# Kernel optimization log

Measured on AMD Instinct MI355X. Metric: run time of the kernel, lower is better.

The kernel has to match this reference:

```python
import jax, jax.numpy as jnp
import numpy as np

N_MEL = 80
PRENET = 256
ENC = 512
ARNN = 1024
DRNN = 1024
ATT = 128
NF = 32
K = 31
B, S, T = 16, 256, 400


def _lstm_cell(x, h, c, Wih, Whh, bih, bhh):
    # torch nn.LSTMCell math: gates ordered i, f, g, o
    z = x @ Wih.T + bih + h @ Whh.T + bhh
    i, f, g, o = jnp.split(z, 4, axis=-1)
    c_new = jax.nn.sigmoid(f) * c + jax.nn.sigmoid(i) * jnp.tanh(g)
    h_new = jax.nn.sigmoid(o) * jnp.tanh(c_new)
    return h_new, c_new


def setup_inputs() -> dict:
    key = jax.random.key(0)
    ks = jax.random.split(key, 24)
    g = lambda i, shape: (jax.random.normal(ks[i], shape, jnp.float32) * 0.02)
    inp = {
        'memory': jax.random.normal(ks[0], (B, S, ENC), jnp.float32),
        'decoder_inputs': jax.random.normal(ks[1], (B, N_MEL, T), jnp.float32),
        # prenet (LinearNorm, no bias in tacotron2 prenet)
        'Wpre1': g(2, (PRENET, N_MEL)),
        'Wpre2': g(3, (PRENET, PRENET)),
        # attention LSTMCell: input = prenet + enc = 256 + 512 = 768
        'Wih_a': g(4, (4 * ARNN, PRENET + ENC)),
        'Whh_a': g(5, (4 * ARNN, ARNN)),
        'bih_a': jnp.zeros((4 * ARNN,), jnp.float32),
        'bhh_a': jnp.zeros((4 * ARNN,), jnp.float32),
        # location-sensitive attention
        'Wq': g(6, (ATT, ARNN)),
        'Wm': g(7, (ATT, ENC)),
        'v': g(8, (ATT,)),
        'Wloc_conv': g(9, (NF, 2, K)),
        'Wloc_dense': g(10, (ATT, NF)),
        # decoder LSTMCell: input = att_rnn + enc = 1024 + 512 = 1536
        'Wih_d': g(11, (4 * DRNN, ARNN + ENC)),
        'Whh_d': g(12, (4 * DRNN, DRNN)),
        'bih_d': jnp.zeros((4 * DRNN,), jnp.float32),
        'bhh_d': jnp.zeros((4 * DRNN,), jnp.float32),
        # projections from [decoder_hidden ; context] = 1536
        'Wproj': g(13, (N_MEL, DRNN + ENC)),
        'bproj': jnp.zeros((N_MEL,), jnp.float32),
        'Wgate': g(14, (1, DRNN + ENC)),
        'bgate': jnp.zeros((1,), jnp.float32),
        'memory_lengths': jax.random.randint(ks[15], (B,), S // 2, S + 1),
    }
    return inp


def reference(memory, decoder_inputs, Wpre1, Wpre2, Wih_a, Whh_a, bih_a, bhh_a,
              Wq, Wm, v, Wloc_conv, Wloc_dense, Wih_d, Whh_d, bih_d, bhh_d,
              Wproj, bproj, Wgate, bgate, memory_lengths):
    # pad mask: True where position is beyond the encoder length
    pad_mask = jnp.arange(S)[None, :] >= memory_lengths[:, None]  # [B,S]
    proc_mem = memory @ Wm.T  # [B,S,ATT], memory_layer precomputed once

    # parse_decoder_inputs + go frame: [B,80,T] -> [T,B,80], prepend zeros
    di = jnp.transpose(decoder_inputs, (2, 0, 1))
    di = jnp.concatenate([jnp.zeros((1, B, N_MEL), di.dtype), di], axis=0)
    # prenet (dropout treated as identity for deterministic reference)
    pre = jax.nn.relu(jax.nn.relu(di @ Wpre1.T) @ Wpre2.T)  # [T+1,B,256]
    xs = pre[:-1]  # loop consumes indices 0..T-1

    carry0 = (jnp.zeros((B, ARNN)), jnp.zeros((B, ARNN)),
              jnp.zeros((B, DRNN)), jnp.zeros((B, DRNN)),
              jnp.zeros((B, S)), jnp.zeros((B, S)), jnp.zeros((B, ENC)))

    def step(carry, x):
        ah, ac, dh, dc, aw, awc, ctx = carry
        ah, ac = _lstm_cell(jnp.concatenate([x, ctx], -1), ah, ac,
                            Wih_a, Whh_a, bih_a, bhh_a)
        # location features from [prev_weights ; cum_weights]
        awcat = jnp.stack([aw, awc], axis=1)  # [B,2,S]
        loc = jax.lax.conv_general_dilated(
            awcat, Wloc_conv, (1,), ((K // 2, K // 2),),
            dimension_numbers=('NCH', 'OIH', 'NCH'))  # [B,NF,S]
        proc_att = jnp.einsum('bfs,af->bsa', loc, Wloc_dense)  # [B,S,ATT]
        q = ah @ Wq.T  # [B,ATT]
        e = jnp.tanh(q[:, None, :] + proc_att + proc_mem) @ v  # [B,S]
        e = jnp.where(pad_mask, -1e9, e)
        aw = jax.nn.softmax(e, axis=-1)
        ctx = jnp.einsum('bs,bse->be', aw, memory)  # [B,ENC]
        awc = awc + aw
        dh, dc = _lstm_cell(jnp.concatenate([ah, ctx], -1), dh, dc,
                            Wih_d, Whh_d, bih_d, bhh_d)
        hac = jnp.concatenate([dh, ctx], -1)  # [B,1536]
        mel = hac @ Wproj.T + bproj  # [B,80]
        gate = (hac @ Wgate.T + bgate)[:, 0]  # [B]
        return (ah, ac, dh, dc, aw, awc, ctx), (mel, gate, aw)

    _, (mels, gates, aligns) = jax.lax.scan(step, carry0, xs)
    mel_outputs = jnp.transpose(mels, (1, 2, 0))  # [B,80,T]
    gate_outputs = gates.T  # [B,T]
    alignments = jnp.transpose(aligns, (1, 0, 2))  # [B,T,S]
    return mel_outputs, gate_outputs, alignments
```

## Files before the change

### kernel.cpp

```cpp
#include <hip/hip_runtime.h>

typedef unsigned short ushort_t;
typedef unsigned int uint_t;
typedef float f32x4_t __attribute__((ext_vector_type(4)));
typedef short bf16x8_t __attribute__((ext_vector_type(8)));

#define NBATCH 16
#define SMEM   256
#define TSTEPS 400

#define F_XSB   0u
#define F_PM    819200u
#define F_MMIX  1343488u
#define F_W1T   1675264u
#define F_W2T   1695744u
#define F_AHB   1761280u
#define F_DHB   1777664u
#define F_CTXB  1794048u
#define F_DHF   1802240u
#define F_AWG   1835008u
#define F_FLG   1851392u
#define ZERO_BASE  F_AHB
#define ZERO_COUNT 95616u

#define AHF  0
#define CTXF 64
#define DHFL 192
#define AWF  320
#define PRF  336

#define A_AH    0
#define A_CTX   32768
#define A_XS    49152
#define A_RED   57344
#define D_AH    0
#define D_CTX   32768
#define D_DH    49152
#define D_MEMU  81920
#define D_COMB  114688
#define D_AWSM  120832
#define D_PART  121856
#define T_AH    0
#define T_LOCU  32768
#define T_QSM   53248
#define T_VSM   53760
#define T_ESM   54272
#define T_RED   55296
#define T_SMAW  55424
#define T_SMAWC 56448
#define P_DHP   0
#define P_AWP   65536
#define SMEM_BYTES 123904

struct Ptrs {
  const float *memory, *dec_in, *Wpre1, *Wpre2, *Wih_a, *Whh_a, *bih_a, *bhh_a,
              *Wq, *Wm, *v, *Wc, *Wld, *Wih_d, *Whh_d, *bih_d, *bhh_d,
              *Wproj, *bproj, *Wgate, *bgate;
  const int *mlen;
  float *ws;
  float *out;
};

__device__ __forceinline__ float ftanh(float x) {
  float e = __expf(2.f * x);
  return 1.f - 2.f / (e + 1.f);
}
__device__ __forceinline__ float fsig(float x) { return 1.f / (1.f + __expf(-x)); }

__device__ __forceinline__ unsigned f2bfbits(float x) {
  unsigned u = __builtin_bit_cast(unsigned, x);
  return (u + 0x7FFFu + ((u >> 16) & 1u)) >> 16;
}
__device__ __forceinline__ float bf2f(ushort_t u) {
  unsigned v = ((unsigned)u) << 16;
  return __builtin_bit_cast(float, v);
}
__device__ __forceinline__ bf16x8_t packbf8(const float* f) {
  bf16x8_t r;
#pragma unroll
  for (int j = 0; j < 8; ++j) r[j] = (short)f2bfbits(f[j]);
  return r;
}
__device__ __forceinline__ bf16x8_t pack_from_f4(const float* src) {
  const float4* s4 = (const float4*)src;
  float4 lo = s4[0], hi = s4[1];
  float tmp[8] = {lo.x, lo.y, lo.z, lo.w, hi.x, hi.y, hi.z, hi.w};
  return packbf8(tmp);
}
__device__ __forceinline__ bf16x8_t ldbf8(const ushort_t* p) {
  return *(const bf16x8_t*)p;
}
__device__ __forceinline__ unsigned long long ldull_a(const unsigned long long* p) {
  return __hip_atomic_load(p, __ATOMIC_RELAXED, __HIP_MEMORY_SCOPE_AGENT);
}
__device__ __forceinline__ void stull_a(unsigned long long* p, unsigned long long v) {
  __hip_atomic_store(p, v, __ATOMIC_RELAXED, __HIP_MEMORY_SCOPE_AGENT);
}
__device__ __forceinline__ void stf_a(float* p, float v) {
  __hip_atomic_store(p, v, __ATOMIC_RELAXED, __HIP_MEMORY_SCOPE_AGENT);
}
__device__ __forceinline__ float ldf_a(const float* p) {
  return __hip_atomic_load(p, __ATOMIC_RELAXED, __HIP_MEMORY_SCOPE_AGENT);
}
__device__ __forceinline__ void pollge(int* flg, int slot, int thr) {
  while (__hip_atomic_load(flg + slot * 16, __ATOMIC_RELAXED, __HIP_MEMORY_SCOPE_AGENT) < thr)
    __builtin_amdgcn_s_sleep(1);
}
__device__ __forceinline__ void sig(int* flg, int slot, int val) {
  __hip_atomic_store(flg + slot * 16, val, __ATOMIC_RELAXED, __HIP_MEMORY_SCOPE_AGENT);
}
__device__ __forceinline__ void lds_st8(char* smc, int base, int row, int row_sh,
                                        int bytecol, unsigned long long v) {
  *(unsigned long long*)(smc + base + (row << row_sh) + (bytecol ^ ((row & 7) << 4))) = v;
}
__device__ __forceinline__ bf16x8_t lds_bf8(const char* smc, int base, int row,
                                            int row_sh, int bytecol) {
  return *(const bf16x8_t*)(smc + base + (row << row_sh) + (bytecol ^ ((row & 7) << 4)));
}
#define MFMA16(a,b,c) __builtin_amdgcn_mfma_f32_16x16x32_bf16((a),(b),(c),0,0,0)

__global__ __launch_bounds__(256) void k_zero(Ptrs p) {
  unsigned i = blockIdx.x * 256 + threadIdx.x;
  if (i < ZERO_COUNT) p.ws[ZERO_BASE + i] = 0.f;
}

__global__ __launch_bounds__(256) void k_transpose(Ptrs p) {
  int i = blockIdx.x * 256 + threadIdx.x;
  if (i < 20480) {
    int m = i >> 8, c = i & 255;
    p.ws[F_W1T + i] = p.Wpre1[c * 80 + m];
  } else if (i < 20480 + 65536) {
    int j = i - 20480;
    int pp = j >> 8, q = j & 255;
    p.ws[F_W2T + j] = p.Wpre2[q * 256 + pp];
  }
}

__global__ __launch_bounds__(256) void k_prenet(Ptrs p) {
  __shared__ float dil[NBATCH * 80];
  __shared__ float h1[NBATCH * 256];
  const int t = blockIdx.x, tid = threadIdx.x;
  const float* W1T = p.ws + F_W1T;
  const float* W2T = p.ws + F_W2T;

  for (int i = tid; i < NBATCH * 80; i += 256) {
    int b = i / 80, m = i - b * 80;
    dil[i] = (t == 0) ? 0.f : p.dec_in[((size_t)b * 80 + m) * 400 + (t - 1)];
  }
  __syncthreads();

  float acc[NBATCH];
#pragma unroll
  for (int b = 0; b < NBATCH; ++b) acc[b] = 0.f;
  for (int m = 0; m < 80; ++m) {
    float w = W1T[m * 256 + tid];
#pragma unroll
    for (int b = 0; b < NBATCH; ++b) acc[b] = fmaf(dil[b * 80 + m], w, acc[b]);
  }
#pragma unroll
  for (int b = 0; b < NBATCH; ++b) h1[b * 256 + tid] = fmaxf(acc[b], 0.f);
  __syncthreads();

#pragma unroll
  for (int b = 0; b < NBATCH; ++b) acc[b] = 0.f;
  for (int q = 0; q < 256; ++q) {
    float w = W2T[q * 256 + tid];
#pragma unroll
    for (int b = 0; b < NBATCH; ++b) acc[b] = fmaf(h1[b * 256 + q], w, acc[b]);
  }
  ushort_t* xsbU = (ushort_t*)(p.ws + F_XSB);
#pragma unroll
  for (int b = 0; b < NBATCH; ++b)
    xsbU[((size_t)(t * NBATCH + b)) * 256 + tid] = (ushort_t)f2bfbits(fmaxf(acc[b], 0.f));
}

__global__ __launch_bounds__(256) void k_packwq(Ptrs p) {
  int s = blockIdx.x * 256 + threadIdx.x;
  if (s >= 16384) return;
  int m16s = s & 15, kqs = (s >> 4) & 3, c = (s >> 6) & 31, w = s >> 11;
  int r = w * 16 + m16s, col = c * 32 + kqs * 8;
  ushort_t* wqp = (ushort_t*)(p.ws + F_W1T);
  bf16x8_t f = pack_from_f4(p.Wq + (size_t)r * 1024 + col);
  *(bf16x8_t*)(wqp + (size_t)s * 8) = f;
}

__global__ __launch_bounds__(256) void k_procmem(Ptrs p) {
  __shared__ alignas(16) float msl[16 * 512];
  const int b = blockIdx.x >> 4, s0 = (blockIdx.x & 15) << 4;
  const int tid = threadIdx.x;
  const float4* src = (const float4*)(p.memory + ((size_t)(b * SMEM + s0)) * 512);
  float4* dst = (float4*)msl;
  for (int i = tid; i < 16 * 512 / 4; i += 256) dst[i] = src[i];
  __syncthreads();

  const int a = tid & 127, sg = tid >> 7;
  const float4* wm = (const float4*)(p.Wm + (size_t)a * 512);
  float* pm = p.ws + F_PM;
  float acc[8];
#pragma unroll
  for (int j = 0; j < 8; ++j) acc[j] = 0.f;
  for (int k = 0; k < 128; ++k) {
    float4 w = wm[k];
#pragma unroll
    for (int j = 0; j < 8; ++j) {
      float4 m = ((const float4*)(msl + (size_t)(sg * 8 + j) * 512))[k];
      acc[j] += w.x * m.x + w.y * m.y + w.z * m.z + w.w * m.w;
    }
  }
#pragma unroll
  for (int j = 0; j < 8; ++j)
    pm[((size_t)(b * SMEM + s0 + sg * 8 + j)) * 128 + a] = acc[j];
}

__global__ __launch_bounds__(512) void k_premix(Ptrs p) {
  const int b = blockIdx.x, tid = threadIdx.x;
  float* M = p.ws + F_MMIX;
  for (int i = tid; i < 81 * 256; i += 512) {
    int row = i >> 8, s = i & 255;
    const float* wrow = (row < 80) ? p.Wproj + (size_t)row * 1536 + 1024 : p.Wgate + 1024;
    const float4* w4 = (const float4*)wrow;
    const float4* m4 = (const float4*)(p.memory + ((size_t)(b * 256 + s)) * 512);
    float acc = 0.f;
#pragma unroll 4
    for (int k = 0; k < 128; ++k) {
      float4 w = w4[k], m = m4[k];
      acc += w.x * m.x + w.y * m.y + w.z * m.z + w.w * m.w;
    }
    M[((size_t)b * 81 + row) * 256 + s] = acc;
  }
}

__global__ __launch_bounds__(512, 1) void k_scan(Ptrs p) {
  extern __shared__ char smc[];
  const int bid = blockIdx.x, tid = threadIdx.x;
  const int wid = tid >> 6, lane = tid & 63;
  const int m16 = lane & 15, kq = lane >> 4;

  float* ws = p.ws;
  ushort_t* xsbU  = (ushort_t*)(ws + F_XSB);
  float*    pmF   = ws + F_PM;
  float*    Mx    = ws + F_MMIX;
  unsigned long long* ahb8 = (unsigned long long*)(ws + F_AHB);
  unsigned long long* dhb8 = (unsigned long long*)(ws + F_DHB);
  unsigned long long* ctxb8 = (unsigned long long*)(ws + F_CTXB);
  float*    dhfF  = ws + F_DHF;
  float*    awGF  = ws + F_AWG;
  int*      flg   = (int*)(ws + F_FLG);
  float* out_mel  = p.out;
  float* out_gate = p.out + 512000;
  float* out_al   = p.out + 518400;

  if (bid < 64) {
    const int ls = wid >> 1, half = wid & 1;
    const int strip = (bid << 2) | ls;
    const int gA = m16 & 3, jA = m16 >> 2;
    const int wrowA = gA * 1024 + strip * 4 + jA;
    bf16x8_t wA[28];
#pragma unroll
    for (int c = 0; c < 28; ++c) {
      int k0 = (half * 28 + c) * 32 + kq * 8;
      const float* src = (k0 < 768) ? p.Wih_a + (size_t)wrowA * 768 + k0
                                    : p.Whh_a + (size_t)wrowA * 1024 + (k0 - 768);
      wA[c] = pack_from_f4(src);
    }
    const int nnA = strip * 4 + kq;
    float biasA[4];
#pragma unroll
    for (int r = 0; r < 4; ++r) biasA[r] = p.bih_a[r * 1024 + nnA] + p.bhh_a[r * 1024 + nnA];
    float acState = 0.f;
    float* ared = (float*)(smc + A_RED);
    __syncthreads();

    for (int t = 0; t < TSTEPS; ++t) {
      const int pc = t & 1, pp = (t + 1) & 1;
      if (tid < 64) pollge(flg, AHF + tid, t);
      else if (tid < 192) pollge(flg, CTXF + tid - 64, t);
      __syncthreads();

      {
        const unsigned long long* ag = ahb8 + (size_t)pp * 4096;
        const unsigned long long* cg = ctxb8 + (size_t)pp * 2048;
        const unsigned long long* xg = (const unsigned long long*)xsbU + (size_t)t * 1024;
        unsigned long long tA[8], tC[4], tX[2];
#pragma unroll
        for (int i = 0; i < 8; ++i) tA[i] = ldull_a(ag + tid + i * 512);
#pragma unroll
        for (int i = 0; i < 4; ++i) tC[i] = ldull_a(cg + tid + i * 512);
#pragma unroll
        for (int i = 0; i < 2; ++i) tX[i] = xg[tid + i * 512];
#pragma unroll
        for (int i = 0; i < 8; ++i) { int u = tid + i * 512; lds_st8(smc, A_AH, u >> 8, 11, (u & 255) * 8, tA[i]); }
#pragma unroll
        for (int i = 0; i < 4; ++i) { int u = tid + i * 512; lds_st8(smc, A_CTX, u >> 7, 10, (u & 127) * 8, tC[i]); }
#pragma unroll
        for (int i = 0; i < 2; ++i) { int u = tid + i * 512; lds_st8(smc, A_XS, u >> 6, 9, (u & 63) * 8, tX[i]); }
      }
      __syncthreads();

      f32x4_t a0 = {0,0,0,0}, a1 = {0,0,0,0};
      if (half == 0) {
#pragma unroll
        for (int c = 0; c < 28; ++c) {
          bf16x8_t bf;
          if (c < 8)       bf = lds_bf8(smc, A_XS,  m16, 9,  c * 64 + kq * 16);
          else if (c < 24) bf = lds_bf8(smc, A_CTX, m16, 10, (c - 8) * 64 + kq * 16);
          else             bf = lds_bf8(smc, A_AH,  m16, 11, (c - 24) * 64 + kq * 16);
          if (c & 1) a1 = MFMA16(wA[c], bf, a1); else a0 = MFMA16(wA[c], bf, a0);
        }
      } else {
#pragma unroll
        for (int c = 0; c < 28; ++c) {
          bf16x8_t bf = lds_bf8(smc, A_AH, m16, 11, (4 + c) * 64 + kq * 16);
          if (c & 1) a1 = MFMA16(wA[c], bf, a1); else a0 = MFMA16(wA[c], bf, a0);
        }
#pragma unroll
        for (int r = 0; r < 4; ++r) ared[((ls * 64 + lane) << 2) + r] = a0[r] + a1[r];
      }
      __syncthreads();
      if (half == 0) {
        float z[4];
#pragma unroll
        for (int r = 0; r < 4; ++r)
          z[r] = a0[r] + a1[r] + ared[((ls * 64 + lane) << 2) + r] + biasA[r];
        float cn = fsig(z[1]) * acState + fsig(z[0]) * ftanh(z[2]);
        acState = cn;
        float h = fsig(z[3]) * ftanh(cn);
        unsigned hb = f2bfbits(h);
        unsigned b0 = __shfl(hb, m16);
        unsigned b1 = __shfl(hb, m16 + 16);
        unsigned b2 = __shfl(hb, m16 + 32);
        unsigned b3 = __shfl(hb, m16 + 48);
        if (kq == 0) {
          unsigned long long u = (unsigned long long)(b0 | (b1 << 16))
                               | ((unsigned long long)(b2 | (b3 << 16)) << 32);
          stull_a(ahb8 + ((size_t)(pc * 16 + m16)) * 256 + strip, u);
        }
      }
      __syncthreads();
      if (tid == 0) sig(flg, AHF + bid, t + 1);
    }
  } else if (bid < 192) {
    const int ls = wid >> 2, qt = wid & 3;
    const int strip = ((bid - 64) << 1) | ls;
    const int gD = m16 & 3, jD = m16 >> 2;
    const int wrowD = gD * 1024 + strip * 4 + jD;
    bf16x8_t wD[20];
#pragma unroll
    for (int c = 0; c < 20; ++c) {
      int k0 = (qt * 20 + c) * 32 + kq * 8;
      const float* src = (k0 < 1536) ? p.Wih_d + (size_t)wrowD * 1536 + k0
                                     : p.Whh_d + (size_t)wrowD * 1024 + (k0 - 1536);
      wD[c] = pack_from_f4(src);
    }
    const int nnD = strip * 4 + kq;
    float biasD[4];
#pragma unroll
    for (int r = 0; r < 4; ++r) biasD[r] = p.bih_d[r * 1024 + nnD] + p.bhh_d[r * 1024 + nnD];
    float dcState = 0.f;

    const int cb = (bid - 64) >> 3, sl = (bid - 64) & 7;
    float* comb = (float*)(smc + D_COMB);
    float* awsm = (float*)(smc + D_AWSM);
    float* part = (float*)(smc + D_PART);
    ushort_t* memu = (ushort_t*)(smc + D_MEMU);
    for (int i = tid; i < 16384; i += 512) {
      int s = i >> 6, c = i & 63;
      memu[i] = (ushort_t)f2bfbits(p.memory[((size_t)cb * 256 + s) * 512 + sl * 64 + c]);
    }
    __syncthreads();

    for (int t = 0; t <= TSTEPS; ++t) {
      const int pc = t & 1, pw = (t + 1) & 1;
      if (t >= 1) {
        if (tid < 64) pollge(flg, AHF + tid, t);
        else if (tid < 192) pollge(flg, CTXF + tid - 64, t);
        else if (tid < 320) pollge(flg, DHFL + tid - 192, t - 1);
        else if (tid < 328) pollge(flg, PRF + tid - 320, t - 2);
        __syncthreads();

        {
          const unsigned long long* ag = ahb8 + (size_t)pw * 4096;
          const unsigned long long* cg = ctxb8 + (size_t)pw * 2048;
          const unsigned long long* dg = dhb8 + (size_t)pc * 4096;
          unsigned long long tA[8], tC[4], tD[8];
#pragma unroll
          for (int i = 0; i < 8; ++i) tA[i] = ldull_a(ag + tid + i * 512);
#pragma unroll
          for (int i = 0; i < 4; ++i) tC[i] = ldull_a(cg + tid + i * 512);
#pragma unroll
          for (int i = 0; i < 8; ++i) tD[i] = ldull_a(dg + tid + i * 512);
#pragma unroll
          for (int i = 0; i < 8; ++i) { int u = tid + i * 512; lds_st8(smc, D_AH, u >> 8, 11, (u & 255) * 8, tA[i]); }
#pragma unroll
          for (int i = 0; i < 4; ++i) { int u = tid + i * 512; lds_st8(smc, D_CTX, u >> 7, 10, (u & 127) * 8, tC[i]); }
#pragma unroll
          for (int i = 0; i < 8; ++i) { int u = tid + i * 512; lds_st8(smc, D_DH, u >> 8, 11, (u & 255) * 8, tD[i]); }
        }
        __syncthreads();

        f32x4_t a0 = {0,0,0,0}, a1 = {0,0,0,0};
#define DFRAG_AH(ch)  lds_bf8(smc, D_AH,  m16, 11, (ch) * 64 + kq * 16)
#define DFRAG_CTX(ch) lds_bf8(smc, D_CTX, m16, 10, (ch) * 64 + kq * 16)
#define DFRAG_DH(ch)  lds_bf8(smc, D_DH,  m16, 11, (ch) * 64 + kq * 16)
#define DMFMA(BF) { bf16x8_t bf = (BF); \
          if (c & 1) a1 = MFMA16(wD[c], bf, a1); else a0 = MFMA16(wD[c], bf, a0); }
        if (qt == 0) {
#pragma unroll
          for (int c = 0; c < 20; ++c) DMFMA(DFRAG_AH(c))
        } else if (qt == 1) {
#pragma unroll
          for (int c = 0; c < 20; ++c) { if (c < 12) DMFMA(DFRAG_AH(20 + c)) else DMFMA(DFRAG_CTX(c - 12)) }
        } else if (qt == 2) {
#pragma unroll
          for (int c = 0; c < 20; ++c) { if (c < 8) DMFMA(DFRAG_CTX(8 + c)) else DMFMA(DFRAG_DH(c - 8)) }
        } else {
#pragma unroll
          for (int c = 0; c < 20; ++c) DMFMA(DFRAG_DH(12 + c))
        }
#undef DMFMA
        if (qt != 0) {
#pragma unroll
          for (int r = 0; r < 4; ++r)
            comb[(((ls * 3 + qt - 1) * 64 + lane) << 2) + r] = a0[r] + a1[r];
        }
        __syncthreads();
        if (qt == 0) {
          float z[4];
#pragma unroll
          for (int r = 0; r < 4; ++r) {
            z[r] = a0[r] + a1[r] + biasD[r];
#pragma unroll
            for (int j = 0; j < 3; ++j) z[r] += comb[(((ls * 3 + j) * 64 + lane) << 2) + r];
          }
          float cn = fsig(z[1]) * dcState + fsig(z[0]) * ftanh(z[2]);
          dcState = cn;
          float h = fsig(z[3]) * ftanh(cn);
          stf_a(dhfF + (size_t)pw * 16384 + m16 * 1024 + nnD, h);
          unsigned hb = f2bfbits(h);
          unsigned b0 = __shfl(hb, m16);
          unsigned b1 = __shfl(hb, m16 + 16);
          unsigned b2 = __shfl(hb, m16 + 32);
          unsigned b3 = __shfl(hb, m16 + 48);
          if (kq == 0) {
            unsigned long long u = (unsigned long long)(b0 | (b1 << 16))
                                 | ((unsigned long long)(b2 | (b3 << 16)) << 32);
            stull_a(dhb8 + ((size_t)(pw * 16 + m16)) * 256 + strip, u);
          }
        }
        __syncthreads();
        if (tid == 0) sig(flg, DHFL + (bid - 64), t);
      }
      if (t < TSTEPS) {
        if (tid == 0) pollge(flg, AWF + cb, t + 1);
        __syncthreads();
        if (tid < 256) awsm[tid] = ldf_a(awGF + (size_t)(t & 3) * 4096 + cb * 256 + tid);
        __syncthreads();
        const int c = tid & 63, sg = tid >> 6;
        float acc = 0.f;
#pragma unroll 8
        for (int si = 0; si < 32; ++si) {
          int s = sg * 32 + si;
          acc = fmaf(awsm[s], bf2f(memu[s * 64 + c]), acc);
        }
        part[sg * 64 + c] = acc;
        __syncthreads();
        if (tid < 64) {
          float v = 0.f;
#pragma unroll
          for (int j = 0; j < 8; ++j) v += part[j * 64 + tid];
          unsigned vb = f2bfbits(v);
          int base = tid & ~3;
          unsigned c0 = __shfl(vb, base);
          unsigned c1 = __shfl(vb, base + 1);
          unsigned c2 = __shfl(vb, base + 2);
          unsigned c3 = __shfl(vb, base + 3);
          if ((tid & 3) == 0) {
            unsigned long long u = (unsigned long long)(c0 | (c1 << 16))
                                 | ((unsigned long long)(c2 | (c3 << 16)) << 32);
            stull_a(ctxb8 + ((size_t)(pc * 16 + cb)) * 128 + ((sl * 64 + tid) >> 2), u);
          }
        }
        __syncthreads();
        if (tid == 0) sig(flg, CTXF + (bid - 64), t + 1);
      }
    }
  } else if (bid < 208) {
    const int b = bid - 192;
    const int mlenb = p.mlen[b];
    ushort_t* locu = (ushort_t*)(smc + T_LOCU);
    float* qsm   = (float*)(smc + T_QSM);
    float* vsm   = (float*)(smc + T_VSM);
    float* esm   = (float*)(smc + T_ESM);
    float* red   = (float*)(smc + T_RED);
    float* smaw  = (float*)(smc + T_SMAW);
    float* smawc = (float*)(smc + T_SMAWC);
    const ushort_t* wqp = (const ushort_t*)(ws + F_W1T);

    bf16x8_t wLd[8];
#pragma unroll
    for (int at = 0; at < 8; ++at)
      wLd[at] = pack_from_f4(p.Wld + ((size_t)(at * 16 + m16)) * 32 + kq * 8);
    bf16x8_t wC[2][2];
#pragma unroll
    for (int ft = 0; ft < 2; ++ft)
#pragma unroll
      for (int ck = 0; ck < 2; ++ck) {
        float tmp[8];
#pragma unroll
        for (int jj = 0; jj < 8; ++jj) {
          int k2 = ck * 32 + kq * 8 + jj;
          float vv = 0.f;
          if (k2 < 62) { int ch = (k2 < 31) ? 0 : 1; int k = k2 - 31 * ch;
            vv = p.Wc[((size_t)(ft * 16 + m16) * 2 + ch) * 31 + k]; }
          tmp[jj] = vv;
        }
        wC[ft][ck] = packbf8(tmp);
      }
    uint_t pmreg[2][8][2];
#pragma unroll
    for (int u = 0; u < 2; ++u) {
      int sloc = (wid * 2 + u) * 16 + m16;
#pragma unroll
      for (int at = 0; at < 8; ++at)
#pragma unroll
        for (int rp = 0; rp < 2; ++rp) {
          const float* src = pmF + ((size_t)(b * 256 + sloc)) * 128 + at * 16 + kq * 4 + rp * 2;
          pmreg[u][at][rp] = f2bfbits(src[0]) | (f2bfbits(src[1]) << 16);
        }
    }
    if (tid < 128) vsm[tid] = p.v[tid];
    if (tid < 256) { smaw[tid] = 0.f; smawc[tid] = 0.f; }
    __syncthreads();

    for (int t = 0; t < TSTEPS; ++t) {
      const int pc = t & 1;
#pragma unroll
      for (int u = 0; u < 4; ++u) {
        int task = wid * 4 + u;
        int stile = task >> 1, ft = task & 1;
        int scol = stile * 16 + m16;
        f32x4_t acc = {0,0,0,0};
#pragma unroll
        for (int ck = 0; ck < 2; ++ck) {
          float tmp[8];
#pragma unroll
          for (int jj = 0; jj < 8; ++jj) {
            int k2 = ck * 32 + kq * 8 + jj;
            float vv = 0.f;
            if (k2 < 62) {
              int ch = (k2 < 31) ? 0 : 1; int k = k2 - 31 * ch;
              int sp = scol + k - 15;
              if (sp >= 0 && sp < 256) vv = (ch ? smawc : smaw)[sp];
            }
            tmp[jj] = vv;
          }
          acc = MFMA16(wC[ft][ck], packbf8(tmp), acc);
        }
#pragma unroll
        for (int r = 0; r < 4; ++r)
          locu[scol * 40 + ft * 16 + kq * 4 + r] = (ushort_t)f2bfbits(acc[r]);
      }
      if (tid < 64) pollge(flg, AHF + tid, t + 1);
      else if (tid < 72) pollge(flg, PRF + (tid - 64), t - 3);
      __syncthreads();
      {
        const unsigned long long* ag = ahb8 + (size_t)pc * 4096;
        unsigned long long tA[8];
#pragma unroll
        for (int i = 0; i < 8; ++i) tA[i] = ldull_a(ag + tid + i * 512);
#pragma unroll
        for (int i = 0; i < 8; ++i) { int u = tid + i * 512; lds_st8(smc, T_AH, u >> 8, 11, (u & 255) * 8, tA[i]); }
      }
      __syncthreads();
      {
        f32x4_t acc = {0,0,0,0};
#pragma unroll
        for (int c = 0; c < 32; ++c) {
          bf16x8_t wf = ldbf8(wqp + (((size_t)(wid * 32 + c)) * 64 + lane) * 8);
          bf16x8_t hf = lds_bf8(smc, T_AH, m16, 11, c * 64 + kq * 16);
          acc = MFMA16(wf, hf, acc);
        }
        if (m16 == b) {
#pragma unroll
          for (int r = 0; r < 4; ++r) qsm[wid * 16 + kq * 4 + r] = acc[r];
        }
      }
      __syncthreads();
#pragma unroll
      for (int u = 0; u < 2; ++u) {
        int sloc = (wid * 2 + u) * 16 + m16;
        bf16x8_t Bfrag = ldbf8(locu + sloc * 40 + kq * 8);
        float eacc = 0.f;
#pragma unroll
        for (int at = 0; at < 8; ++at) {
          f32x4_t C = {0,0,0,0};
          C = MFMA16(wLd[at], Bfrag, C);
#pragma unroll
          for (int r = 0; r < 4; ++r) {
            int a = at * 16 + kq * 4 + r;
            uint_t pw_ = pmreg[u][at][r >> 1];
            float pmv = bf2f((ushort_t)((r & 1) ? (pw_ >> 16) : (pw_ & 0xFFFF)));
            eacc = fmaf(vsm[a], ftanh(C[r] + qsm[a] + pmv), eacc);
          }
        }
        eacc += __shfl_xor(eacc, 16);
        eacc += __shfl_xor(eacc, 32);
        if (sloc >= mlenb) eacc = -1.0e9f;
        if (kq == 0) esm[sloc] = eacc;
      }
      __syncthreads();
      float ev = 0.f;
      if (tid < 256) {
        ev = esm[tid];
        float mv = ev;
        for (int o = 32; o; o >>= 1) mv = fmaxf(mv, __shfl_xor(mv, o));
        if (lane == 0) red[wid] = mv;
      }
      __syncthreads();
      float gmax = fmaxf(fmaxf(red[0], red[1]), fmaxf(red[2], red[3]));
      float pv = 0.f;
      if (tid < 256) {
        pv = __expf(ev - gmax);
        float sv = pv;
        for (int o = 32; o; o >>= 1) sv += __shfl_xor(sv, o);
        if (lane == 0) red[8 + wid] = sv;
      }
      __syncthreads();
      float gsum = red[8] + red[9] + red[10] + red[11];
      float awv = 0.f;
      if (tid < 256) {
        awv = pv / gsum;
        smaw[tid] = awv;
        smawc[tid] += awv;
        stf_a(awGF + (size_t)(t & 3) * 4096 + b * 256 + tid, awv);
      }
      __syncthreads();
      if (tid == 0) sig(flg, AWF + b, t + 1);
      if (tid < 256) out_al[((size_t)b * 400 + t) * 256 + tid] = awv;
    }
  } else if (bid < 216) {
    const int wv = (bid - 208) * 8 + wid;
    int rows[2] = {wv * 2, wv * 2 + 1};
    float wdh[2][16], mreg[2][16][4], biasr[2];
#pragma unroll
    for (int rr = 0; rr < 2; ++rr) {
      int row = rows[rr];
      biasr[rr] = 0.f;
#pragma unroll
      for (int j = 0; j < 16; ++j) wdh[rr][j] = 0.f;
#pragma unroll
      for (int b2 = 0; b2 < 16; ++b2)
#pragma unroll
        for (int j = 0; j < 4; ++j) mreg[rr][b2][j] = 0.f;
      if (row <= 80) {
        const float* wsrc = (row < 80) ? p.Wproj + (size_t)row * 1536 : p.Wgate;
#pragma unroll
        for (int j = 0; j < 16; ++j) wdh[rr][j] = wsrc[lane + 64 * j];
        biasr[rr] = (row < 80) ? p.bproj[row] : p.bgate[0];
#pragma unroll
        for (int b2 = 0; b2 < 16; ++b2)
#pragma unroll
          for (int j = 0; j < 4; ++j)
            mreg[rr][b2][j] = Mx[((size_t)b2 * 81 + row) * 256 + lane + 64 * j];
      }
    }
    float* dhp = (float*)(smc + P_DHP);
    float* awp = (float*)(smc + P_AWP);
    __syncthreads();
    for (int t = 1; t <= TSTEPS; ++t) {
      const int pw = (t + 1) & 1;
      if (tid < 128) pollge(flg, DHFL + tid, t);
      else if (tid < 144) pollge(flg, AWF + tid - 128, t);
      __syncthreads();
      {
        const unsigned long long* ag = (const unsigned long long*)(awGF + (size_t)((t - 1) & 3) * 4096);
        const unsigned long long* dg = (const unsigned long long*)(dhfF + (size_t)pw * 16384);
        unsigned long long tw[4], td[16];
#pragma unroll
        for (int i = 0; i < 4; ++i) tw[i] = ldull_a(ag + tid + i * 512);
#pragma unroll
        for (int i = 0; i < 16; ++i) td[i] = ldull_a(dg + tid + i * 512);
#pragma unroll
        for (int i = 0; i < 4; ++i) ((unsigned long long*)awp)[tid + i * 512] = tw[i];
#pragma unroll
        for (int i = 0; i < 16; ++i) ((unsigned long long*)dhp)[tid + i * 512] = td[i];
      }
      __syncthreads();
      if (wv <= 40) {
        for (int b2 = 0; b2 < 16; ++b2) {
          float h[16];
#pragma unroll
          for (int j = 0; j < 16; ++j) h[j] = dhp[b2 * 1024 + lane + 64 * j];
#pragma unroll
          for (int rr = 0; rr < 2; ++rr) {
            if (rows[rr] > 80) continue;
            float d = 0.f;
#pragma unroll
            for (int j = 0; j < 16; ++j) d = fmaf(wdh[rr][j], h[j], d);
#pragma unroll
            for (int j = 0; j < 4; ++j) d = fmaf(mreg[rr][b2][j], awp[b2 * 256 + lane + 64 * j], d);
            for (int o = 32; o; o >>= 1) d += __shfl_xor(d, o);
            if (lane == 0) {
              d += biasr[rr];
              if (rows[rr] < 80) out_mel[((size_t)b2 * 80 + rows[rr]) * 400 + (t - 1)] = d;
              else out_gate[(size_t)b2 * 400 + (t - 1)] = d;
            }
          }
        }
      }
      __syncthreads();
      if (tid == 0) sig(flg, PRF + (bid - 208), t);
    }
  }
}

extern "C" void kernel_launch(void* const* d_in, const int* in_sizes, int n_in,
                              void* d_out, int out_size, void* d_ws, size_t ws_size,
                              hipStream_t stream) {
  (void)in_sizes; (void)n_in; (void)out_size; (void)ws_size;
  Ptrs p;
  p.memory = (const float*)d_in[0];
  p.dec_in = (const float*)d_in[1];
  p.Wpre1  = (const float*)d_in[2];
  p.Wpre2  = (const float*)d_in[3];
  p.Wih_a  = (const float*)d_in[4];
  p.Whh_a  = (const float*)d_in[5];
  p.bih_a  = (const float*)d_in[6];
  p.bhh_a  = (const float*)d_in[7];
  p.Wq     = (const float*)d_in[8];
  p.Wm     = (const float*)d_in[9];
  p.v      = (const float*)d_in[10];
  p.Wc     = (const float*)d_in[11];
  p.Wld    = (const float*)d_in[12];
  p.Wih_d  = (const float*)d_in[13];
  p.Whh_d  = (const float*)d_in[14];
  p.bih_d  = (const float*)d_in[15];
  p.bhh_d  = (const float*)d_in[16];
  p.Wproj  = (const float*)d_in[17];
  p.bproj  = (const float*)d_in[18];
  p.Wgate  = (const float*)d_in[19];
  p.bgate  = (const float*)d_in[20];
  p.mlen   = (const int*)d_in[21];
  p.ws  = (float*)d_ws;
  p.out = (float*)d_out;

  static bool attr_done = false;
  if (!attr_done) {
    hipFuncSetAttribute((const void*)k_scan,
                        hipFuncAttributeMaxDynamicSharedMemorySize, SMEM_BYTES);
    attr_done = true;
  }

  hipLaunchKernelGGL(k_zero,      dim3((ZERO_COUNT + 255) / 256), dim3(256), 0, stream, p);
  hipLaunchKernelGGL(k_transpose, dim3(336), dim3(256), 0, stream, p);
  hipLaunchKernelGGL(k_prenet,    dim3(400), dim3(256), 0, stream, p);
  hipLaunchKernelGGL(k_packwq,    dim3(64),  dim3(256), 0, stream, p);
  hipLaunchKernelGGL(k_procmem,   dim3(256), dim3(256), 0, stream, p);
  hipLaunchKernelGGL(k_premix,    dim3(16),  dim3(512), 0, stream, p);
  hipLaunchKernelGGL(k_scan,      dim3(256), dim3(512), SMEM_BYTES, stream, p);
}
```

Before: 8.788 ms.

## Move context computation to dedicated blocks and fuse query projection into attention-LSTM blocks

New measurement: 8.617 ms. Within noise of the previous version (-1.9%).

```diff
diff --git a/kernel.cpp b/kernel.cpp
--- a/kernel.cpp
+++ b/kernel.cpp
@@ -22,6 +22,7 @@
 #define F_FLG   1851392u
 #define ZERO_BASE  F_AHB
 #define ZERO_COUNT 95616u
+#define F_QP    1856896u
 
 #define AHF  0
 #define CTXF 64
@@ -33,24 +34,26 @@
 #define A_CTX   32768
 #define A_XS    49152
 #define A_RED   57344
+#define A_QWQ   61440
+#define A_QH    69632
 #define D_AH    0
 #define D_CTX   32768
 #define D_DH    49152
-#define D_MEMU  81920
-#define D_COMB  114688
-#define D_AWSM  120832
-#define D_PART  121856
-#define T_AH    0
-#define T_LOCU  32768
-#define T_QSM   53248
-#define T_VSM   53760
-#define T_ESM   54272
-#define T_RED   55296
-#define T_SMAW  55424
-#define T_SMAWC 56448
+#define D_COMB  81920
+#define T_LOCU  0
+#define T_QSM   20480
+#define T_VSM   20992
+#define T_ESM   21504
+#define T_RED   22528
+#define T_SMAW  22784
+#define T_SMAWC 23808
+#define T_QRED  24832
+#define C_MEM   0
+#define C_PART  131072
+#define C_AWS   135168
 #define P_DHP   0
 #define P_AWP   65536
-#define SMEM_BYTES 123904
+#define SMEM_BYTES 136192
 
 struct Ptrs {
   const float *memory, *dec_in, *Wpre1, *Wpre2, *Wih_a, *Whh_a, *bih_a, *bhh_a,
@@ -172,16 +175,6 @@
 #pragma unroll
   for (int b = 0; b < NBATCH; ++b)
     xsbU[((size_t)(t * NBATCH + b)) * 256 + tid] = (ushort_t)f2bfbits(fmaxf(acc[b], 0.f));
-}
-
-__global__ __launch_bounds__(256) void k_packwq(Ptrs p) {
-  int s = blockIdx.x * 256 + threadIdx.x;
-  if (s >= 16384) return;
-  int m16s = s & 15, kqs = (s >> 4) & 3, c = (s >> 6) & 31, w = s >> 11;
-  int r = w * 16 + m16s, col = c * 32 + kqs * 8;
-  ushort_t* wqp = (ushort_t*)(p.ws + F_W1T);
-  bf16x8_t f = pack_from_f4(p.Wq + (size_t)r * 1024 + col);
-  *(bf16x8_t*)(wqp + (size_t)s * 8) = f;
 }
 
 __global__ __launch_bounds__(256) void k_procmem(Ptrs p) {
@@ -245,6 +238,7 @@
   unsigned long long* ctxb8 = (unsigned long long*)(ws + F_CTXB);
   float*    dhfF  = ws + F_DHF;
   float*    awGF  = ws + F_AWG;
+  float*    qpF   = ws + F_QP;
   int*      flg   = (int*)(ws + F_FLG);
   float* out_mel  = p.out;
   float* out_gate = p.out + 512000;
@@ -269,31 +263,41 @@
     for (int r = 0; r < 4; ++r) biasA[r] = p.bih_a[r * 1024 + nnA] + p.bhh_a[r * 1024 + nnA];
     float acState = 0.f;
     float* ared = (float*)(smc + A_RED);
+    float* qwq  = (float*)(smc + A_QWQ);
+    float* qh   = (float*)(smc + A_QH);
+    for (int i = tid; i < 2048; i += 512) {
+      int a = i >> 4, c = i & 15;
+      qwq[i] = p.Wq[(size_t)a * 1024 + bid * 16 + c];
+    }
     __syncthreads();
 
     for (int t = 0; t < TSTEPS; ++t) {
       const int pc = t & 1, pp = (t + 1) & 1;
       if (tid < 64) pollge(flg, AHF + tid, t);
-      else if (tid < 192) pollge(flg, CTXF + tid - 64, t);
-      __syncthreads();
-
+      else if (tid >= 96 && tid < 224) pollge(flg, DHFL + (tid - 96), t - 1);
+      __syncthreads();
       {
         const unsigned long long* ag = ahb8 + (size_t)pp * 4096;
+        const unsigned long long* xg = (const unsigned long long*)xsbU + (size_t)t * 1024;
+        unsigned long long tA[8], tX[2];
+#pragma unroll
+        for (int i = 0; i < 8; ++i) tA[i] = ldull_a(ag + tid + i * 512);
+#pragma unroll
+        for (int i = 0; i < 2; ++i) tX[i] = xg[tid + i * 512];
+#pragma unroll
+        for (int i = 0; i < 8; ++i) { int u = tid + i * 512; lds_st8(smc, A_AH, u >> 8, 11, (u & 255) * 8, tA[i]); }
+#pragma unroll
+        for (int i = 0; i < 2; ++i) { int u = tid + i * 512; lds_st8(smc, A_XS, u >> 6, 9, (u & 63) * 8, tX[i]); }
+      }
+      if (tid >= 64 && tid < 96) pollge(flg, CTXF + (tid - 64), t);
+      __syncthreads();
+      {
         const unsigned long long* cg = ctxb8 + (size_t)pp * 2048;
-        const unsigned long long* xg = (const unsigned long long*)xsbU + (size_t)t * 1024;
-        unsigned long long tA[8], tC[4], tX[2];
-#pragma unroll
-        for (int i = 0; i < 8; ++i) tA[i] = ldull_a(ag + tid + i * 512);
+        unsigned long long tC[4];
 #pragma unroll
         for (int i = 0; i < 4; ++i) tC[i] = ldull_a(cg + tid + i * 512);
 #pragma unroll
-        for (int i = 0; i < 2; ++i) tX[i] = xg[tid + i * 512];
-#pragma unroll
-        for (int i = 0; i < 8; ++i) { int u = tid + i * 512; lds_st8(smc, A_AH, u >> 8, 11, (u & 255) * 8, tA[i]); }
-#pragma unroll
         for (int i = 0; i < 4; ++i) { int u = tid + i * 512; lds_st8(smc, A_CTX, u >> 7, 10, (u & 127) * 8, tC[i]); }
-#pragma unroll
-        for (int i = 0; i < 2; ++i) { int u = tid + i * 512; lds_st8(smc, A_XS, u >> 6, 9, (u & 63) * 8, tX[i]); }
       }
       __syncthreads();
 
@@ -325,6 +329,7 @@
         float cn = fsig(z[1]) * acState + fsig(z[0]) * ftanh(z[2]);
         acState = cn;
         float h = fsig(z[3]) * ftanh(cn);
+        qh[(m16 << 4) + ls * 4 + kq] = h;
         unsigned hb = f2bfbits(h);
         unsigned b0 = __shfl(hb, m16);
         unsigned b1 = __shfl(hb, m16 + 16);
@@ -337,6 +342,25 @@
         }
       }
       __syncthreads();
+      {
+        int a = tid & 127, bg = tid >> 7;
+        const float* wrow = qwq + a * 16;
+        float s0 = 0.f, s1 = 0.f, s2 = 0.f, s3 = 0.f;
+#pragma unroll
+        for (int c = 0; c < 16; ++c) {
+          float wv = wrow[c];
+          s0 = fmaf(wv, qh[((bg * 4 + 0) << 4) + c], s0);
+          s1 = fmaf(wv, qh[((bg * 4 + 1) << 4) + c], s1);
+          s2 = fmaf(wv, qh[((bg * 4 + 2) << 4) + c], s2);
+          s3 = fmaf(wv, qh[((bg * 4 + 3) << 4) + c], s3);
+        }
+        float* qps = qpF + (size_t)pc * 131072 + bid * 2048 + a;
+        stf_a(qps + (size_t)(bg * 4 + 0) * 128, s0);
+        stf_a(qps + (size_t)(bg * 4 + 1) * 128, s1);
+        stf_a(qps + (size_t)(bg * 4 + 2) * 128, s2);
+        stf_a(qps + (size_t)(bg * 4 + 3) * 128, s3);
+      }
+      __syncthreads();
       if (tid == 0) sig(flg, AHF + bid, t + 1);
     }
   } else if (bid < 192) {
@@ -357,132 +381,91 @@
 #pragma unroll
     for (int r = 0; r < 4; ++r) biasD[r] = p.bih_d[r * 1024 + nnD] + p.bhh_d[r * 1024 + nnD];
     float dcState = 0.f;
-
-    const int cb = (bid - 64) >> 3, sl = (bid - 64) & 7;
     float* comb = (float*)(smc + D_COMB);
-    float* awsm = (float*)(smc + D_AWSM);
-    float* part = (float*)(smc + D_PART);
-    ushort_t* memu = (ushort_t*)(smc + D_MEMU);
-    for (int i = tid; i < 16384; i += 512) {
-      int s = i >> 6, c = i & 63;
-      memu[i] = (ushort_t)f2bfbits(p.memory[((size_t)cb * 256 + s) * 512 + sl * 64 + c]);
-    }
     __syncthreads();
 
-    for (int t = 0; t <= TSTEPS; ++t) {
+    for (int t = 1; t <= TSTEPS; ++t) {
       const int pc = t & 1, pw = (t + 1) & 1;
-      if (t >= 1) {
-        if (tid < 64) pollge(flg, AHF + tid, t);
-        else if (tid < 192) pollge(flg, CTXF + tid - 64, t);
-        else if (tid < 320) pollge(flg, DHFL + tid - 192, t - 1);
-        else if (tid < 328) pollge(flg, PRF + tid - 320, t - 2);
-        __syncthreads();
-
-        {
-          const unsigned long long* ag = ahb8 + (size_t)pw * 4096;
-          const unsigned long long* cg = ctxb8 + (size_t)pw * 2048;
-          const unsigned long long* dg = dhb8 + (size_t)pc * 4096;
-          unsigned long long tA[8], tC[4], tD[8];
-#pragma unroll
-          for (int i = 0; i < 8; ++i) tA[i] = ldull_a(ag + tid + i * 512);
-#pragma unroll
-          for (int i = 0; i < 4; ++i) tC[i] = ldull_a(cg + tid + i * 512);
-#pragma unroll
-          for (int i = 0; i < 8; ++i) tD[i] = ldull_a(dg + tid + i * 512);
-#pragma unroll
-          for (int i = 0; i < 8; ++i) { int u = tid + i * 512; lds_st8(smc, D_AH, u >> 8, 11, (u & 255) * 8, tA[i]); }
-#pragma unroll
-          for (int i = 0; i < 4; ++i) { int u = tid + i * 512; lds_st8(smc, D_CTX, u >> 7, 10, (u & 127) * 8, tC[i]); }
-#pragma unroll
-          for (int i = 0; i < 8; ++i) { int u = tid + i * 512; lds_st8(smc, D_DH, u >> 8, 11, (u & 255) * 8, tD[i]); }
-        }
-        __syncthreads();
-
-        f32x4_t a0 = {0,0,0,0}, a1 = {0,0,0,0};
+      if (tid < 64) pollge(flg, AHF + tid, t);
+      else if (tid >= 96 && tid < 224) pollge(flg, DHFL + (tid - 96), t - 1);
+      else if (tid >= 224 && tid < 232) pollge(flg, PRF + (tid - 224), t - 2);
+      __syncthreads();
+      {
+        const unsigned long long* ag = ahb8 + (size_t)pw * 4096;
+        const unsigned long long* dg = dhb8 + (size_t)pc * 4096;
+        unsigned long long tA[8], tD[8];
+#pragma unroll
+        for (int i = 0; i < 8; ++i) tA[i] = ldull_a(ag + tid + i * 512);
+#pragma unroll
+        for (int i = 0; i < 8; ++i) tD[i] = ldull_a(dg + tid + i * 512);
+#pragma unroll
+        for (int i = 0; i < 8; ++i) { int u = tid + i * 512; lds_st8(smc, D_AH, u >> 8, 11, (u & 255) * 8, tA[i]); }
+#pragma unroll
+        for (int i = 0; i < 8; ++i) { int u = tid + i * 512; lds_st8(smc, D_DH, u >> 8, 11, (u & 255) * 8, tD[i]); }
+      }
+      if (tid >= 64 && tid < 96) pollge(flg, CTXF + (tid - 64), t);
+      __syncthreads();
+      {
+        const unsigned long long* cg = ctxb8 + (size_t)pw * 2048;
+        unsigned long long tC[4];
+#pragma unroll
+        for (int i = 0; i < 4; ++i) tC[i] = ldull_a(cg + tid + i * 512);
+#pragma unroll
+        for (int i = 0; i < 4; ++i) { int u = tid + i * 512; lds_st8(smc, D_CTX, u >> 7, 10, (u & 127) * 8, tC[i]); }
+      }
+      __syncthreads();
+
+      f32x4_t a0 = {0,0,0,0}, a1 = {0,0,0,0};
 #define DFRAG_AH(ch)  lds_bf8(smc, D_AH,  m16, 11, (ch) * 64 + kq * 16)
 #define DFRAG_CTX(ch) lds_bf8(smc, D_CTX, m16, 10, (ch) * 64 + kq * 16)
 #define DFRAG_DH(ch)  lds_bf8(smc, D_DH,  m16, 11, (ch) * 64 + kq * 16)
 #define DMFMA(BF) { bf16x8_t bf = (BF); \
-          if (c & 1) a1 = MFMA16(wD[c], bf, a1); else a0 = MFMA16(wD[c], bf, a0); }
-        if (qt == 0) {
-#pragma unroll
-          for (int c = 0; c < 20; ++c) DMFMA(DFRAG_AH(c))
-        } else if (qt == 1) {
-#pragma unroll
-          for (int c = 0; c < 20; ++c) { if (c < 12) DMFMA(DFRAG_AH(20 + c)) else DMFMA(DFRAG_CTX(c - 12)) }
-        } else if (qt == 2) {
-#pragma unroll
-          for (int c = 0; c < 20; ++c) { if (c < 8) DMFMA(DFRAG_CTX(8 + c)) else DMFMA(DFRAG_DH(c - 8)) }
-        } else {
-#pragma unroll
-          for (int c = 0; c < 20; ++c) DMFMA(DFRAG_DH(12 + c))
-        }
+        if (c & 1) a1 = MFMA16(wD[c], bf, a1); else a0 = MFMA16(wD[c], bf, a0); }
+      if (qt == 0) {
+#pragma unroll
+        for (int c = 0; c < 20; ++c) DMFMA(DFRAG_AH(c))
+      } else if (qt == 1) {
+#pragma unroll
+        for (int c = 0; c < 20; ++c) { if (c < 12) DMFMA(DFRAG_AH(20 + c)) else DMFMA(DFRAG_CTX(c - 12)) }
+      } else if (qt == 2) {
+#pragma unroll
+        for (int c = 0; c < 20; ++c) { if (c < 8) DMFMA(DFRAG_CTX(8 + c)) else DMFMA(DFRAG_DH(c - 8)) }
+      } else {
+#pragma unroll
+        for (int c = 0; c < 20; ++c) DMFMA(DFRAG_DH(12 + c))
+      }
 #undef DMFMA
-        if (qt != 0) {
-#pragma unroll
-          for (int r = 0; r < 4; ++r)
-            comb[(((ls * 3 + qt - 1) * 64 + lane) << 2) + r] = a0[r] + a1[r];
-        }
-        __syncthreads();
-        if (qt == 0) {
-          float z[4];
-#pragma unroll
-          for (int r = 0; r < 4; ++r) {
-            z[r] = a0[r] + a1[r] + biasD[r];
-#pragma unroll
-            for (int j = 0; j < 3; ++j) z[r] += comb[(((ls * 3 + j) * 64 + lane) << 2) + r];
-          }
-          float cn = fsig(z[1]) * dcState + fsig(z[0]) * ftanh(z[2]);
-          dcState = cn;
-          float h = fsig(z[3]) * ftanh(cn);
-          stf_a(dhfF + (size_t)pw * 16384 + m16 * 1024 + nnD, h);
-          unsigned hb = f2bfbits(h);
-          unsigned b0 = __shfl(hb, m16);
-          unsigned b1 = __shfl(hb, m16 + 16);
-          unsigned b2 = __shfl(hb, m16 + 32);
-          unsigned b3 = __shfl(hb, m16 + 48);
-          if (kq == 0) {
-            unsigned long long u = (unsigned long long)(b0 | (b1 << 16))
-                                 | ((unsigned long long)(b2 | (b3 << 16)) << 32);
-            stull_a(dhb8 + ((size_t)(pw * 16 + m16)) * 256 + strip, u);
-          }
-        }
-        __syncthreads();
-        if (tid == 0) sig(flg, DHFL + (bid - 64), t);
-      }
-      if (t < TSTEPS) {
-        if (tid == 0) pollge(flg, AWF + cb, t + 1);
-        __syncthreads();
-        if (tid < 256) awsm[tid] = ldf_a(awGF + (size_t)(t & 3) * 4096 + cb * 256 + tid);
-        __syncthreads();
-        const int c = tid & 63, sg = tid >> 6;
-        float acc = 0.f;
-#pragma unroll 8
-        for (int si = 0; si < 32; ++si) {
-          int s = sg * 32 + si;
-          acc = fmaf(awsm[s], bf2f(memu[s * 64 + c]), acc);
-        }
-        part[sg * 64 + c] = acc;
-        __syncthreads();
-        if (tid < 64) {
-          float v = 0.f;
-#pragma unroll
-          for (int j = 0; j < 8; ++j) v += part[j * 64 + tid];
-          unsigned vb = f2bfbits(v);
-          int base = tid & ~3;
-          unsigned c0 = __shfl(vb, base);
-          unsigned c1 = __shfl(vb, base + 1);
-          unsigned c2 = __shfl(vb, base + 2);
-          unsigned c3 = __shfl(vb, base + 3);
-          if ((tid & 3) == 0) {
-            unsigned long long u = (unsigned long long)(c0 | (c1 << 16))
-                                 | ((unsigned long long)(c2 | (c3 << 16)) << 32);
-            stull_a(ctxb8 + ((size_t)(pc * 16 + cb)) * 128 + ((sl * 64 + tid) >> 2), u);
-          }
-        }
-        __syncthreads();
-        if (tid == 0) sig(flg, CTXF + (bid - 64), t + 1);
-      }
+      if (qt != 0) {
+#pragma unroll
+        for (int r = 0; r < 4; ++r)
+          comb[(((ls * 3 + qt - 1) * 64 + lane) << 2) + r] = a0[r] + a1[r];
+      }
+      __syncthreads();
+      if (qt == 0) {
+        float z[4];
+#pragma unroll
+        for (int r = 0; r < 4; ++r) {
+          z[r] = a0[r] + a1[r] + biasD[r];
+#pragma unroll
+          for (int j = 0; j < 3; ++j) z[r] += comb[(((ls * 3 + j) * 64 + lane) << 2) + r];
+        }
+        float cn = fsig(z[1]) * dcState + fsig(z[0]) * ftanh(z[2]);
+        dcState = cn;
+        float h = fsig(z[3]) * ftanh(cn);
+        stf_a(dhfF + (size_t)pw * 16384 + m16 * 1024 + nnD, h);
+        unsigned hb = f2bfbits(h);
+        unsigned b0 = __shfl(hb, m16);
+        unsigned b1 = __shfl(hb, m16 + 16);
+        unsigned b2 = __shfl(hb, m16 + 32);
+        unsigned b3 = __shfl(hb, m16 + 48);
+        if (kq == 0) {
+          unsigned long long u = (unsigned long long)(b0 | (b1 << 16))
+                               | ((unsigned long long)(b2 | (b3 << 16)) << 32);
+          stull_a(dhb8 + ((size_t)(pw * 16 + m16)) * 256 + strip, u);
+        }
+      }
+      __syncthreads();
+      if (tid == 0) sig(flg, DHFL + (bid - 64), t);
     }
   } else if (bid < 208) {
     const int b = bid - 192;
@@ -494,7 +477,7 @@
     float* red   = (float*)(smc + T_RED);
     float* smaw  = (float*)(smc + T_SMAW);
     float* smawc = (float*)(smc + T_SMAWC);
-    const ushort_t* wqp = (const ushort_t*)(ws + F_W1T);
+    float* qred  = (float*)(smc + T_QRED);
 
     bf16x8_t wLd[8];
 #pragma unroll
@@ -533,7 +516,6 @@
     __syncthreads();
 
     for (int t = 0; t < TSTEPS; ++t) {
-      const int pc = t & 1;
 #pragma unroll
       for (int u = 0; u < 4; ++u) {
         int task = wid * 4 + u;
@@ -564,27 +546,16 @@
       else if (tid < 72) pollge(flg, PRF + (tid - 64), t - 3);
       __syncthreads();
       {
-        const unsigned long long* ag = ahb8 + (size_t)pc * 4096;
-        unsigned long long tA[8];
-#pragma unroll
-        for (int i = 0; i < 8; ++i) tA[i] = ldull_a(ag + tid + i * 512);
-#pragma unroll
-        for (int i = 0; i < 8; ++i) { int u = tid + i * 512; lds_st8(smc, T_AH, u >> 8, 11, (u & 255) * 8, tA[i]); }
-      }
-      __syncthreads();
-      {
-        f32x4_t acc = {0,0,0,0};
-#pragma unroll
-        for (int c = 0; c < 32; ++c) {
-          bf16x8_t wf = ldbf8(wqp + (((size_t)(wid * 32 + c)) * 64 + lane) * 8);
-          bf16x8_t hf = lds_bf8(smc, T_AH, m16, 11, c * 64 + kq * 16);
-          acc = MFMA16(wf, hf, acc);
-        }
-        if (m16 == b) {
-#pragma unroll
-          for (int r = 0; r < 4; ++r) qsm[wid * 16 + kq * 4 + r] = acc[r];
-        }
-      }
+        int a = tid & 127, g = tid >> 7;
+        const float* qps = qpF + (size_t)(t & 1) * 131072 + b * 128 + a;
+        float s = 0.f;
+#pragma unroll
+        for (int k = 0; k < 16; ++k)
+          s += ldf_a(qps + (size_t)(g * 16 + k) * 2048);
+        qred[g * 128 + a] = s;
+      }
+      __syncthreads();
+      if (tid < 128) qsm[tid] = qred[tid] + qred[128 + tid] + qred[256 + tid] + qred[384 + tid];
       __syncthreads();
 #pragma unroll
       for (int u = 0; u < 2; ++u) {
@@ -710,6 +681,60 @@
       }
       __syncthreads();
       if (tid == 0) sig(flg, PRF + (bid - 208), t);
+    }
+  } else if (bid < 248) {
+    const int cbid = bid - 216;
+    const int b = cbid >> 1, half2 = cbid & 1;
+    ushort_t* memu2 = (ushort_t*)(smc + C_MEM);
+    float* part = (float*)(smc + C_PART);
+    float* awsm = (float*)(smc + C_AWS);
+    for (int i = tid; i < 16384; i += 512) {
+      int s = i >> 6, c4 = i & 63;
+      float4 m = *(const float4*)(p.memory + ((size_t)(b * 256 + s)) * 512 + half2 * 256 + c4 * 4);
+      ushort_t* dst = memu2 + s * 256 + c4 * 4;
+      dst[0] = (ushort_t)f2bfbits(m.x);
+      dst[1] = (ushort_t)f2bfbits(m.y);
+      dst[2] = (ushort_t)f2bfbits(m.z);
+      dst[3] = (ushort_t)f2bfbits(m.w);
+    }
+    __syncthreads();
+
+    for (int t = 0; t < TSTEPS; ++t) {
+      const int pc = t & 1;
+      if (tid < 64) pollge(flg, AHF + tid, t);
+      else if (tid < 192) pollge(flg, DHFL + (tid - 64), t - 1);
+      else if (tid == 192) pollge(flg, AWF + b, t + 1);
+      __syncthreads();
+      if (tid < 256) awsm[tid] = ldf_a(awGF + (size_t)(t & 3) * 4096 + b * 256 + tid);
+      __syncthreads();
+      const int c = tid & 127, sg = tid >> 7;
+      const uint_t* mrow = (const uint_t*)memu2;
+      float a0 = 0.f, a1 = 0.f;
+#pragma unroll 8
+      for (int si = 0; si < 64; ++si) {
+        int s = sg * 64 + si;
+        uint_t mm = mrow[s * 128 + c];
+        float av = awsm[s];
+        a0 = fmaf(bf2f((ushort_t)(mm & 0xFFFF)), av, a0);
+        a1 = fmaf(bf2f((ushort_t)(mm >> 16)), av, a1);
+      }
+      part[sg * 256 + c * 2] = a0;
+      part[sg * 256 + c * 2 + 1] = a1;
+      __syncthreads();
+      if (tid < 64) {
+        unsigned pk[4];
+#pragma unroll
+        for (int j = 0; j < 4; ++j) {
+          int col = tid * 4 + j;
+          float v = part[col] + part[256 + col] + part[512 + col] + part[768 + col];
+          pk[j] = f2bfbits(v);
+        }
+        unsigned long long u = (unsigned long long)(pk[0] | (pk[1] << 16))
+                             | ((unsigned long long)(pk[2] | (pk[3] << 16)) << 32);
+        stull_a(ctxb8 + ((size_t)(pc * 16 + b)) * 128 + half2 * 64 + tid, u);
+      }
+      __syncthreads();
+      if (tid == 0) sig(flg, CTXF + cbid, t + 1);
     }
   }
 }
@@ -754,7 +779,6 @@
   hipLaunchKernelGGL(k_zero,      dim3((ZERO_COUNT + 255) / 256), dim3(256), 0, stream, p);
   hipLaunchKernelGGL(k_transpose, dim3(336), dim3(256), 0, stream, p);
   hipLaunchKernelGGL(k_prenet,    dim3(400), dim3(256), 0, stream, p);
-  hipLaunchKernelGGL(k_packwq,    dim3(64),  dim3(256), 0, stream, p);
   hipLaunchKernelGGL(k_procmem,   dim3(256), dim3(256), 0, stream, p);
   hipLaunchKernelGGL(k_premix,    dim3(16),  dim3(512), 0, stream, p);
   hipLaunchKernelGGL(k_scan,      dim3(256), dim3(512), SMEM_BYTES, stream, p);
```
